# Optimization experiments

Measured on AMD Instinct MI355X. Metric: run time of the kernel, lower is better.

Reference implementation:

```python
import jax, jax.numpy as jnp
import numpy as np

B, DIM, H, W = 4, 512, 64, 64
HEADS = 8
MAX_FREQ = 10000.0


def _rope_cos_sin(h, w, head_dim, dtype):
    # 2D RoPE: first quarter of half_dim uses row position, second quarter uses col position
    half = head_dim // 2
    quarter = half // 2
    pos_h = jnp.arange(h, dtype=dtype)
    pos_w = jnp.arange(w, dtype=dtype)
    gh, gw = jnp.meshgrid(pos_h, pos_w, indexing='ij')
    pos = jnp.stack([gh.ravel(), gw.ravel()], axis=-1)  # [N, 2]
    freqs = 1.0 / (MAX_FREQ ** (jnp.arange(quarter, dtype=dtype) / quarter))  # [quarter]
    ang_x = pos[:, 0:1] * freqs  # [N, quarter]
    ang_y = pos[:, 1:2] * freqs  # [N, quarter]
    cos = jnp.concatenate([jnp.cos(ang_x), jnp.cos(ang_y)], axis=-1)  # [N, half]
    sin = jnp.concatenate([jnp.sin(ang_x), jnp.sin(ang_y)], axis=-1)  # [N, half]
    return cos, sin


def _apply_rope(x, cos, sin):
    # x: [B, heads, N, head_dim]; cos/sin: [N, head_dim//2]
    d = x.shape[-1] // 2
    x1, x2 = x[..., :d], x[..., d:]
    return jnp.concatenate([x1 * cos - x2 * sin, x1 * sin + x2 * cos], axis=-1)


def setup_inputs() -> dict:
    key = jax.random.key(0)
    kx, kq, kp = jax.random.split(key, 3)
    x = jax.random.normal(kx, (B, DIM, H, W), dtype=jnp.float32)
    w_qkv = jax.random.normal(kq, (3 * DIM, DIM), dtype=jnp.float32) * (DIM ** -0.5)
    w_proj = jax.random.normal(kp, (DIM, DIM), dtype=jnp.float32) * (DIM ** -0.5)
    return {"x": x, "w_qkv": w_qkv, "w_proj": w_proj}


def reference(x, w_qkv, w_proj):
    Bb, C, Hh, Ww = x.shape
    heads = HEADS
    hd = C // heads
    N = Hh * Ww
    # 1x1 conv (bias-free) == channel-wise linear
    qkv = jnp.einsum('bchw,oc->bohw', x, w_qkv)  # [B, 3C, H, W]
    qkv = qkv.reshape(Bb, 3, heads, hd, Hh, Ww).transpose(1, 0, 2, 4, 5, 3)  # [3, B, heads, H, W, hd]
    q = qkv[0].reshape(Bb, heads, N, hd)
    k = qkv[1].reshape(Bb, heads, N, hd)
    v = qkv[2].reshape(Bb, heads, N, hd)
    cos, sin = _rope_cos_sin(Hh, Ww, hd, x.dtype)
    q = _apply_rope(q, cos, sin)
    k = _apply_rope(k, cos, sin)
    scale = hd ** -0.5
    attn = jax.nn.softmax(jnp.einsum('bhnd,bhmd->bhnm', q, k) * scale, axis=-1)  # [B, heads, N, N]
    out = jnp.einsum('bhnm,bhmd->bhnd', attn, v)  # [B, heads, N, hd]
    out = out.reshape(Bb, heads, Hh, Ww, hd).transpose(0, 1, 4, 2, 3).reshape(Bb, C, Hh, Ww)
    return jnp.einsum('bchw,oc->bohw', out, w_proj)
```

## Files before the change

kernel.cpp:

```cpp
#include <hip/hip_runtime.h>
#include <math.h>

#define B_    4
#define CDIM  512
#define HEADS 8
#define HD    64
#define NN    4096
#define QSZ   ((size_t)B_*HEADS*NN*HD)
#define SCALE_Q 0.18033688011112042f

typedef __attribute__((ext_vector_type(8))) short short8;
typedef __attribute__((ext_vector_type(4))) float f32x4;
union U4S8 { uint4 u; short8 s; };

__device__ inline unsigned pk(float a, float b) {
    unsigned ua = __float_as_uint(a), ub = __float_as_uint(b);
    ua += 0x7FFFu + ((ua >> 16) & 1u);
    ub += 0x7FFFu + ((ub >> 16) & 1u);
    return (ua >> 16) | (ub & 0xFFFF0000u);
}
__device__ inline unsigned short bf16_1(float a) {
    unsigned ua = __float_as_uint(a);
    ua += 0x7FFFu + ((ua >> 16) & 1u);
    return (unsigned short)(ua >> 16);
}
__device__ inline unsigned pkru(float a, float b) {
    unsigned ua = __float_as_uint(a) + 0x8000u;
    unsigned ub = __float_as_uint(b) + 0x8000u;
    return __builtin_amdgcn_perm(ub, ua, 0x07060302);
}

__device__ inline void load_lds16(const unsigned short* g, unsigned short* l) {
    __builtin_amdgcn_global_load_lds(
        (const __attribute__((address_space(1))) unsigned int*)g,
        (__attribute__((address_space(3))) unsigned int*)l, 16, 0, 0);
}

__global__ void conv_w_kernel(const float* __restrict__ wq, const float* __restrict__ wp,
                              unsigned short* __restrict__ wqb, unsigned short* __restrict__ wpb) {
    int id = blockIdx.x * 256 + threadIdx.x;
    const float* src; unsigned short* dst; size_t off; float sc = 1.0f;
    if (id < 98304) { src = wq; dst = wqb; off = (size_t)id * 8; if (off < 262144) sc = SCALE_Q; }
    else            { src = wp; dst = wpb; off = (size_t)(id - 98304) * 8; }
    float4 a = *(const float4*)(src + off);
    float4 b = *(const float4*)(src + off + 4);
    uint4 u;
    u.x = pk(a.x * sc, a.y * sc); u.y = pk(a.z * sc, a.w * sc);
    u.z = pk(b.x * sc, b.y * sc); u.w = pk(b.z * sc, b.w * sc);
    *(uint4*)(dst + off) = u;
}

__global__ void rope_table_kernel(float* __restrict__ ct, float* __restrict__ st) {
    int id = blockIdx.x * 256 + threadIdx.x;
    int j = id >> 12, n = id & 4095;
    int i = j & 15;
    float pos = (j < 16) ? (float)(n >> 6) : (float)(n & 63);
    float freq = exp2f(-(float)i * 0.8304820237218406f);
    float ang = pos * freq;
    ct[id] = cosf(ang);
    st[id] = sinf(ang);
}

__global__ __launch_bounds__(256) void transpose_x_kernel(
        const float* __restrict__ x, unsigned short* __restrict__ xt) {
    __shared__ unsigned short T[64 * 72];
    int t = threadIdx.x;
    int b = blockIdx.z, c0 = blockIdx.y * 64, n0 = blockIdx.x * 64;
    const float* xb = x + ((size_t)b * CDIM + c0) * NN + n0;
    int crow = t >> 2, nseg = t & 3;
#pragma unroll
    for (int g = 0; g < 4; ++g) {
        float4 f = *(const float4*)(xb + (size_t)crow * NN + nseg * 16 + g * 4);
        int nb = nseg * 16 + g * 4;
        T[(nb + 0) * 72 + crow] = bf16_1(f.x);
        T[(nb + 1) * 72 + crow] = bf16_1(f.y);
        T[(nb + 2) * 72 + crow] = bf16_1(f.z);
        T[(nb + 3) * 72 + crow] = bf16_1(f.w);
    }
    __syncthreads();
    unsigned short* xo = xt + ((size_t)b * NN + n0) * CDIM + c0;
    int nrow = t >> 2, cseg = t & 3;
    uint4 u0 = *(uint4*)(T + nrow * 72 + cseg * 16);
    uint4 u1 = *(uint4*)(T + nrow * 72 + cseg * 16 + 8);
    *(uint4*)(xo + (size_t)nrow * CDIM + cseg * 16)     = u0;
    *(uint4*)(xo + (size_t)nrow * CDIM + cseg * 16 + 8) = u1;
}

__global__ __launch_bounds__(256, 2) void qkv_mfma_kernel(
        const unsigned short* __restrict__ xt, const unsigned short* __restrict__ wq,
        unsigned short* __restrict__ qbf, unsigned short* __restrict__ kbf,
        unsigned short* __restrict__ vt,
        const float* __restrict__ ct, const float* __restrict__ st) {
    __shared__ unsigned short smem[8192];
    int t = threadIdx.x;
    int lane = t & 63, w = t >> 6;
    int qlo = lane & 15, quad = lane >> 4;
    int b = blockIdx.z, o0 = blockIdx.y * 128, n0 = blockIdx.x * 128;
    const unsigned short* xb = xt + (size_t)b * NN * CDIM;
    int row = t >> 2, seg = t & 3;
    int wn = (w & 1) * 64, wo = (w >> 1) * 64;

    f32x4 acc[4][4];
#pragma unroll
    for (int i = 0; i < 4; ++i)
#pragma unroll
        for (int j = 0; j < 4; ++j) acc[i][j] = f32x4{0.f, 0.f, 0.f, 0.f};

    for (int k0 = 0; k0 < 512; k0 += 32) {
        __syncthreads();
        load_lds16(xb + (size_t)(n0 + row) * 512 + k0 + seg * 8,        smem + t * 8);
        load_lds16(xb + (size_t)(n0 + 64 + row) * 512 + k0 + seg * 8,   smem + 2048 + t * 8);
        load_lds16(wq + (size_t)(o0 + row) * 512 + k0 + seg * 8,        smem + 4096 + t * 8);
        load_lds16(wq + (size_t)(o0 + 64 + row) * 512 + k0 + seg * 8,   smem + 6144 + t * 8);
        __syncthreads();
        U4S8 af[4], bf[4];
#pragma unroll
        for (int mt = 0; mt < 4; ++mt)
            af[mt].u = *(const uint4*)(smem + (wn + 16 * mt + qlo) * 32 + quad * 8);
#pragma unroll
        for (int nt = 0; nt < 4; ++nt)
            bf[nt].u = *(const uint4*)(smem + 4096 + (wo + 16 * nt + qlo) * 32 + quad * 8);
#pragma unroll
        for (int mt = 0; mt < 4; ++mt)
#pragma unroll
            for (int nt = 0; nt < 4; ++nt)
                acc[mt][nt] = __builtin_amdgcn_mfma_f32_16x16x32_bf16(
                    af[mt].s, bf[nt].s, acc[mt][nt], 0, 0, 0);
    }

    int og = o0 + wo;
    int s = og >> 9;
    int h = (og & 511) >> 6;
    int bh = b * HEADS + h;
    if (s < 2) {
        unsigned short* dst = (s ? kbf : qbf) + (size_t)bh * NN * HD;
#pragma unroll
        for (int mt = 0; mt < 4; ++mt) {
            int nbase = n0 + wn + 16 * mt + 4 * quad;
#pragma unroll
            for (int ntp = 0; ntp < 2; ++ntp) {
                int j = 16 * ntp + qlo;
                float4 c4 = *(const float4*)(ct + (size_t)j * NN + nbase);
                float4 s4 = *(const float4*)(st + (size_t)j * NN + nbase);
                float cc[4] = {c4.x, c4.y, c4.z, c4.w};
                float ss[4] = {s4.x, s4.y, s4.z, s4.w};
#pragma unroll
                for (int r = 0; r < 4; ++r) {
                    float x1 = acc[mt][ntp][r], x2 = acc[mt][ntp + 2][r];
                    size_t base = (size_t)(nbase + r) * HD;
                    dst[base + j]      = bf16_1(x1 * cc[r] - x2 * ss[r]);
                    dst[base + j + 32] = bf16_1(x1 * ss[r] + x2 * cc[r]);
                }
            }
        }
    } else {
        unsigned short* dst = vt + (size_t)bh * HD * NN;
#pragma unroll
        for (int mt = 0; mt < 4; ++mt)
#pragma unroll
            for (int nt = 0; nt < 4; ++nt) {
                int d = 16 * nt + qlo;
                int n = n0 + wn + 16 * mt + 4 * quad;
                uint2 u;
                u.x = pk(acc[mt][nt][0], acc[mt][nt][1]);
                u.y = pk(acc[mt][nt][2], acc[mt][nt][3]);
                *(uint2*)(dst + (size_t)d * NN + n) = u;
            }
    }
}

__global__ __launch_bounds__(256, 2) void attn_kernel(
        const unsigned short* __restrict__ qbf, const unsigned short* __restrict__ kbf,
        const unsigned short* __restrict__ vt, unsigned short* __restrict__ aot) {
    __shared__ unsigned char smem[18432];
    int t = threadIdx.x;
    int lane = t & 63, w = t >> 6;
    int qlo = lane & 15, quad = lane >> 4;
    int bb = blockIdx.z, hh = blockIdx.y;
    int bh = bb * HEADS + hh;
    int n0w = blockIdx.x * 256 + w * 64;

    U4S8 qf[4][2];
    const unsigned short* qg = qbf + ((size_t)bh * NN + n0w) * HD;
#pragma unroll
    for (int nt = 0; nt < 4; ++nt)
#pragma unroll
        for (int kt = 0; kt < 2; ++kt)
            qf[nt][kt].u = *(const uint4*)(qg + (size_t)(16 * nt + qlo) * 64 + 32 * kt + 8 * quad);

    f32x4 O[4][4];
#pragma unroll
    for (int mt = 0; mt < 4; ++mt)
#pragma unroll
        for (int nt = 0; nt < 4; ++nt) O[mt][nt] = f32x4{0.f, 0.f, 0.f, 0.f};
    float lx[4] = {0.f, 0.f, 0.f, 0.f};
    float ly[4] = {0.f, 0.f, 0.f, 0.f};

    const uint4* kg = (const uint4*)kbf + (size_t)bh * NN * 8;
    const uint4* vg = (const uint4*)vt  + (size_t)bh * 64 * 512;

    int rr0 = t >> 3, s8 = t & 7;
    int voff = (s8 >> 2) * 64 + (s8 & 1) * 32 + ((s8 >> 1) & 1) * 8;
    uint4 kr0, kr1, vr0, vr1;
    kr0 = kg[(size_t)rr0 * 8 + s8];
    kr1 = kg[(size_t)(32 + rr0) * 8 + s8];
    vr0 = vg[(size_t)rr0 * 512 + s8];
    vr1 = vg[(size_t)(32 + rr0) * 512 + s8];

    for (int c = 0; c < NN / 64; ++c) {
        __syncthreads();
        *(uint4*)(smem + rr0 * 144 + s8 * 16)        = kr0;
        *(uint4*)(smem + (32 + rr0) * 144 + s8 * 16) = kr1;
        *(uint2*)(smem + 9216 + rr0 * 144 + voff)            = make_uint2(vr0.x, vr0.y);
        *(uint2*)(smem + 9216 + rr0 * 144 + voff + 16)       = make_uint2(vr0.z, vr0.w);
        *(uint2*)(smem + 9216 + (32 + rr0) * 144 + voff)     = make_uint2(vr1.x, vr1.y);
        *(uint2*)(smem + 9216 + (32 + rr0) * 144 + voff + 16)= make_uint2(vr1.z, vr1.w);
        __syncthreads();
        if (c + 1 < NN / 64) {
            int m0 = (c + 1) * 64;
            kr0 = kg[(size_t)(m0 + rr0) * 8 + s8];
            kr1 = kg[(size_t)(m0 + 32 + rr0) * 8 + s8];
            vr0 = vg[(size_t)rr0 * 512 + (m0 >> 3) + s8];
            vr1 = vg[(size_t)(32 + rr0) * 512 + (m0 >> 3) + s8];
        }

        f32x4 S[4][4];
#pragma unroll
        for (int mt = 0; mt < 4; ++mt)
#pragma unroll
            for (int nt = 0; nt < 4; ++nt) S[mt][nt] = f32x4{0.f, 0.f, 0.f, 0.f};
#pragma unroll
        for (int kt = 0; kt < 2; ++kt) {
            U4S8 ka[4];
#pragma unroll
            for (int mt = 0; mt < 4; ++mt)
                ka[mt].u = *(const uint4*)(smem + (16 * mt + qlo) * 144 + kt * 64 + quad * 16);
#pragma unroll
            for (int nt = 0; nt < 4; ++nt)
#pragma unroll
                for (int mt = 0; mt < 4; ++mt)
                    S[mt][nt] = __builtin_amdgcn_mfma_f32_16x16x32_bf16(
                        ka[mt].s, qf[nt][kt].s, S[mt][nt], 0, 0, 0);
        }

        uint2 pd[4][4];
#pragma unroll
        for (int nt = 0; nt < 4; ++nt)
#pragma unroll
            for (int mt = 0; mt < 4; ++mt) {
                f32x4 s4 = S[mt][nt];
                float p0 = __builtin_amdgcn_exp2f(s4[0]);
                float p1 = __builtin_amdgcn_exp2f(s4[1]);
                float p2 = __builtin_amdgcn_exp2f(s4[2]);
                float p3 = __builtin_amdgcn_exp2f(s4[3]);
                lx[nt] += p0 + p2;
                ly[nt] += p1 + p3;
                pd[nt][mt] = make_uint2(pkru(p0, p1), pkru(p2, p3));
            }

#pragma unroll
        for (int kt = 0; kt < 2; ++kt) {
            U4S8 pa[4];
#pragma unroll
            for (int mtP = 0; mtP < 4; ++mtP)
                pa[mtP].u = make_uint4(pd[mtP][2 * kt].x, pd[mtP][2 * kt].y,
                                       pd[mtP][2 * kt + 1].x, pd[mtP][2 * kt + 1].y);
#pragma unroll
            for (int nt = 0; nt < 4; ++nt) {
                U4S8 vb;
                vb.u = *(const uint4*)(smem + 9216 + (16 * nt + qlo) * 144 + kt * 64 + quad * 16);
#pragma unroll
                for (int mtP = 0; mtP < 4; ++mtP)
                    O[mtP][nt] = __builtin_amdgcn_mfma_f32_16x16x32_bf16(
                        pa[mtP].s, vb.s, O[mtP][nt], 0, 0, 0);
            }
        }
    }

    float linv[4];
#pragma unroll
    for (int nt = 0; nt < 4; ++nt) {
        float l = lx[nt] + ly[nt];
        l += __shfl_xor(l, 16, 64);
        l += __shfl_xor(l, 32, 64);
        linv[nt] = 1.0f / l;
    }
    __syncthreads();
    unsigned short* Tw = (unsigned short*)(smem + w * 4608);
    unsigned short* aob = aot + ((size_t)bb * NN) * CDIM + hh * 64;
#pragma unroll
    for (int mt = 0; mt < 4; ++mt) {
        float iv[4];
#pragma unroll
        for (int r = 0; r < 4; ++r) iv[r] = __shfl(linv[mt], 4 * quad + r, 64);
#pragma unroll
        for (int nt = 0; nt < 4; ++nt)
#pragma unroll
            for (int r = 0; r < 4; ++r)
                Tw[(4 * quad + r) * 72 + 16 * nt + qlo] = bf16_1(O[mt][nt][r] * iv[r]);
        int row = lane >> 2, cseg = lane & 3;
        uint4 u0 = *(uint4*)(Tw + row * 72 + cseg * 16);
        uint4 u1 = *(uint4*)(Tw + row * 72 + cseg * 16 + 8);
        unsigned short* arow = aob + (size_t)(n0w + 16 * mt + row) * CDIM + cseg * 16;
        *(uint4*)(arow)     = u0;
        *(uint4*)(arow + 8) = u1;
    }
}

__global__ __launch_bounds__(256, 2) void proj_mfma_kernel(
        const unsigned short* __restrict__ aot, const unsigned short* __restrict__ wp,
        float* __restrict__ out) {
    __shared__ unsigned short smem[8192];
    int t = threadIdx.x;
    int lane = t & 63, w = t >> 6;
    int qlo = lane & 15, quad = lane >> 4;
    int b = blockIdx.z, o0 = blockIdx.y * 128, n0 = blockIdx.x * 128;
    const unsigned short* ab = aot + (size_t)b * NN * CDIM;
    int row = t >> 2, seg = t & 3;
    int wn = (w & 1) * 64, wo = (w >> 1) * 64;

    f32x4 acc[4][4];
#pragma unroll
    for (int i = 0; i < 4; ++i)
#pragma unroll
        for (int j = 0; j < 4; ++j) acc[i][j] = f32x4{0.f, 0.f, 0.f, 0.f};

    for (int k0 = 0; k0 < 512; k0 += 32) {
        __syncthreads();
        load_lds16(ab + (size_t)(n0 + row) * 512 + k0 + seg * 8,        smem + t * 8);
        load_lds16(ab + (size_t)(n0 + 64 + row) * 512 + k0 + seg * 8,   smem + 2048 + t * 8);
        load_lds16(wp + (size_t)(o0 + row) * 512 + k0 + seg * 8,        smem + 4096 + t * 8);
        load_lds16(wp + (size_t)(o0 + 64 + row) * 512 + k0 + seg * 8,   smem + 6144 + t * 8);
        __syncthreads();
        U4S8 af[4], bf[4];
#pragma unroll
        for (int mt = 0; mt < 4; ++mt)
            af[mt].u = *(const uint4*)(smem + (wn + 16 * mt + qlo) * 32 + quad * 8);
#pragma unroll
        for (int nt = 0; nt < 4; ++nt)
            bf[nt].u = *(const uint4*)(smem + 4096 + (wo + 16 * nt + qlo) * 32 + quad * 8);
#pragma unroll
        for (int mt = 0; mt < 4; ++mt)
#pragma unroll
            for (int nt = 0; nt < 4; ++nt)
                acc[mt][nt] = __builtin_amdgcn_mfma_f32_16x16x32_bf16(
                    af[mt].s, bf[nt].s, acc[mt][nt], 0, 0, 0);
    }

    float* ob = out + (size_t)b * CDIM * NN;
#pragma unroll
    for (int mt = 0; mt < 4; ++mt)
#pragma unroll
        for (int nt = 0; nt < 4; ++nt) {
            int o = o0 + wo + 16 * nt + qlo;
            int n = n0 + wn + 16 * mt + 4 * quad;
            *(float4*)(ob + (size_t)o * NN + n) = *(float4*)&acc[mt][nt];
        }
}

extern "C" void kernel_launch(void* const* d_in, const int* in_sizes, int n_in,
                              void* d_out, int out_size, void* d_ws, size_t ws_size,
                              hipStream_t stream) {
    const float* x      = (const float*)d_in[0];
    const float* w_qkv  = (const float*)d_in[1];
    const float* w_proj = (const float*)d_in[2];
    float* out = (float*)d_out;
    unsigned short* ws = (unsigned short*)d_ws;

    unsigned short* xt  = ws;
    unsigned short* qbf = xt  + QSZ;
    unsigned short* kbf = qbf + QSZ;
    unsigned short* vt  = kbf + QSZ;
    unsigned short* aot = vt  + QSZ;
    unsigned short* wqb = aot + QSZ;
    unsigned short* wpb = wqb + 786432;
    float* ct = (float*)(wpb + 262144);
    float* st = ct + 32 * 4096;

    conv_w_kernel<<<512, 256, 0, stream>>>(w_qkv, w_proj, wqb, wpb);
    rope_table_kernel<<<512, 256, 0, stream>>>(ct, st);
    transpose_x_kernel<<<dim3(64, 8, B_), 256, 0, stream>>>(x, xt);
    qkv_mfma_kernel<<<dim3(32, 12, B_), 256, 0, stream>>>(xt, wqb, qbf, kbf, vt, ct, st);
    attn_kernel<<<dim3(NN / 256, HEADS, B_), 256, 0, stream>>>(qbf, kbf, vt, aot);
    proj_mfma_kernel<<<dim3(32, 4, B_), 256, 0, stream>>>(aot, wpb, out);
}
```

Before: 293.0 us.

## Compute softmax row sums via MFMA with ones vector, use hardware bf16 pack

```diff
diff --git a/kernel.cpp b/kernel.cpp
--- a/kernel.cpp
+++ b/kernel.cpp
@@ -24,10 +24,10 @@
     ua += 0x7FFFu + ((ua >> 16) & 1u);
     return (unsigned short)(ua >> 16);
 }
-__device__ inline unsigned pkru(float a, float b) {
-    unsigned ua = __float_as_uint(a) + 0x8000u;
-    unsigned ub = __float_as_uint(b) + 0x8000u;
-    return __builtin_amdgcn_perm(ub, ua, 0x07060302);
+__device__ inline unsigned cvtpk(float a, float b) {
+    unsigned r;
+    asm("v_cvt_pk_bf16_f32 %0, %1, %2" : "=v"(r) : "v"(a), "v"(b));
+    return r;
 }
 
 __device__ inline void load_lds16(const unsigned short* g, unsigned short* l) {
@@ -188,13 +188,18 @@
         for (int kt = 0; kt < 2; ++kt)
             qf[nt][kt].u = *(const uint4*)(qg + (size_t)(16 * nt + qlo) * 64 + 32 * kt + 8 * quad);
 
+    short8 vone;
+#pragma unroll
+    for (int i = 0; i < 8; ++i) vone[i] = (short)0x3F80;
+
     f32x4 O[4][4];
 #pragma unroll
     for (int mt = 0; mt < 4; ++mt)
 #pragma unroll
         for (int nt = 0; nt < 4; ++nt) O[mt][nt] = f32x4{0.f, 0.f, 0.f, 0.f};
-    float lx[4] = {0.f, 0.f, 0.f, 0.f};
-    float ly[4] = {0.f, 0.f, 0.f, 0.f};
+    f32x4 Lacc[4];
+#pragma unroll
+    for (int mt = 0; mt < 4; ++mt) Lacc[mt] = f32x4{0.f, 0.f, 0.f, 0.f};
 
     const uint4* kg = (const uint4*)kbf + (size_t)bh * NN * 8;
     const uint4* vg = (const uint4*)vt  + (size_t)bh * 64 * 512;
@@ -235,12 +240,14 @@
 #pragma unroll
             for (int mt = 0; mt < 4; ++mt)
                 ka[mt].u = *(const uint4*)(smem + (16 * mt + qlo) * 144 + kt * 64 + quad * 16);
+            __builtin_amdgcn_s_setprio(1);
 #pragma unroll
             for (int nt = 0; nt < 4; ++nt)
 #pragma unroll
                 for (int mt = 0; mt < 4; ++mt)
                     S[mt][nt] = __builtin_amdgcn_mfma_f32_16x16x32_bf16(
                         ka[mt].s, qf[nt][kt].s, S[mt][nt], 0, 0, 0);
+            __builtin_amdgcn_s_setprio(0);
         }
 
         uint2 pd[4][4];
@@ -253,9 +260,7 @@
                 float p1 = __builtin_amdgcn_exp2f(s4[1]);
                 float p2 = __builtin_amdgcn_exp2f(s4[2]);
                 float p3 = __builtin_amdgcn_exp2f(s4[3]);
-                lx[nt] += p0 + p2;
-                ly[nt] += p1 + p3;
-                pd[nt][mt] = make_uint2(pkru(p0, p1), pkru(p2, p3));
+                pd[nt][mt] = make_uint2(cvtpk(p0, p1), cvtpk(p2, p3));
             }
 
 #pragma unroll
@@ -265,6 +270,11 @@
             for (int mtP = 0; mtP < 4; ++mtP)
                 pa[mtP].u = make_uint4(pd[mtP][2 * kt].x, pd[mtP][2 * kt].y,
                                        pd[mtP][2 * kt + 1].x, pd[mtP][2 * kt + 1].y);
+            __builtin_amdgcn_s_setprio(1);
+#pragma unroll
+            for (int mtP = 0; mtP < 4; ++mtP)
+                Lacc[mtP] = __builtin_amdgcn_mfma_f32_16x16x32_bf16(
+                    pa[mtP].s, vone, Lacc[mtP], 0, 0, 0);
 #pragma unroll
             for (int nt = 0; nt < 4; ++nt) {
                 U4S8 vb;
@@ -274,17 +284,10 @@
                     O[mtP][nt] = __builtin_amdgcn_mfma_f32_16x16x32_bf16(
                         pa[mtP].s, vb.s, O[mtP][nt], 0, 0, 0);
             }
-        }
-    }
-
-    float linv[4];
-#pragma unroll
-    for (int nt = 0; nt < 4; ++nt) {
-        float l = lx[nt] + ly[nt];
-        l += __shfl_xor(l, 16, 64);
-        l += __shfl_xor(l, 32, 64);
-        linv[nt] = 1.0f / l;
-    }
+            __builtin_amdgcn_s_setprio(0);
+        }
+    }
+
     __syncthreads();
     unsigned short* Tw = (unsigned short*)(smem + w * 4608);
     unsigned short* aob = aot + ((size_t)bb * NN) * CDIM + hh * 64;
@@ -292,7 +295,7 @@
     for (int mt = 0; mt < 4; ++mt) {
         float iv[4];
 #pragma unroll
-        for (int r = 0; r < 4; ++r) iv[r] = __shfl(linv[mt], 4 * quad + r, 64);
+        for (int r = 0; r < 4; ++r) iv[r] = 1.0f / Lacc[mt][r];
 #pragma unroll
         for (int nt = 0; nt < 4; ++nt)
 #pragma unroll
```

After: 270.6 us. 1.08x faster.
